# Performance work log

Hardware: AMD Instinct MI355X
Metric: run time of the kernel (lower is better)

The kernel has to match this reference:

```python
import jax, jax.numpy as jnp
import numpy as np

IMAGE_SIZE = 800.0          # torchvision default min_size
SCORE_THRESH = 0.25         # box_score_thresh from __init__
NMS_THRESH = 0.5            # box_nms_thresh from __init__
MAX_DET = 100               # torchvision detections_per_img default
BBOX_XFORM_CLIP = float(np.log(1000.0 / 16.0))  # torchvision BoxCoder clamp


def setup_inputs() -> dict:
    key = jax.random.key(0)
    k = jax.random.split(key, 5)
    B, N, D, C = 16, 4000, 1024, 2
    feats = jax.random.normal(k[0], (B, N, D), dtype=jnp.float32)
    # valid proposal boxes (x1,y1,x2,y2) inside the image
    cxcy = jax.random.uniform(k[1], (B, N, 2), minval=64.0, maxval=IMAGE_SIZE - 64.0)
    wh = jax.random.uniform(k[2], (B, N, 2), minval=16.0, maxval=128.0)
    proposals = jnp.concatenate([cxcy - wh * 0.5, cxcy + wh * 0.5], axis=-1)
    W_cls = jax.random.normal(k[3], (C, D), dtype=jnp.float32) * 0.02
    b_cls = jnp.zeros((C,), jnp.float32)
    W_box = jax.random.normal(k[4], (C * 4, D), dtype=jnp.float32) * 0.01
    b_box = jnp.zeros((C * 4,), jnp.float32)
    return dict(feats=feats, proposals=proposals, W_cls=W_cls, b_cls=b_cls,
                W_box=W_box, b_box=b_box)


def _decode_boxes(deltas, proposals):
    # torchvision BoxCoder with weights (10, 10, 5, 5)
    wx, wy, ww, wh = 10.0, 10.0, 5.0, 5.0
    widths = proposals[..., 2] - proposals[..., 0]
    heights = proposals[..., 3] - proposals[..., 1]
    ctr_x = proposals[..., 0] + 0.5 * widths
    ctr_y = proposals[..., 1] + 0.5 * heights
    dx = deltas[..., 0] / wx
    dy = deltas[..., 1] / wy
    dw = jnp.minimum(deltas[..., 2] / ww, BBOX_XFORM_CLIP)
    dh = jnp.minimum(deltas[..., 3] / wh, BBOX_XFORM_CLIP)
    pcx = dx * widths + ctr_x
    pcy = dy * heights + ctr_y
    pw = jnp.exp(dw) * widths
    ph = jnp.exp(dh) * heights
    boxes = jnp.stack([pcx - 0.5 * pw, pcy - 0.5 * ph,
                       pcx + 0.5 * pw, pcy + 0.5 * ph], axis=-1)
    return jnp.clip(boxes, 0.0, IMAGE_SIZE)


def _nms_keep(boxes, scores):
    # greedy NMS for one image; boxes [N,4], scores [N] (already thresholded)
    areas = jnp.maximum(boxes[:, 2] - boxes[:, 0], 0.0) * \
            jnp.maximum(boxes[:, 3] - boxes[:, 1], 0.0)

    def body(carry, _):
        s, keep = carry
        i = jnp.argmax(s)
        valid = s[i] > 0.0
        bi = boxes[i]
        ix1 = jnp.maximum(bi[0], boxes[:, 0])
        iy1 = jnp.maximum(bi[1], boxes[:, 1])
        ix2 = jnp.minimum(bi[2], boxes[:, 2])
        iy2 = jnp.minimum(bi[3], boxes[:, 3])
        inter = jnp.maximum(ix2 - ix1, 0.0) * jnp.maximum(iy2 - iy1, 0.0)
        iou = inter / (areas[i] + areas - inter + 1e-9)
        s = jnp.where(iou > NMS_THRESH, 0.0, s).at[i].set(0.0)
        keep = keep.at[i].set(valid)
        return (s, keep), None

    init = (scores, jnp.zeros(scores.shape, dtype=bool))
    (_, keep), _ = jax.lax.scan(body, init, None, length=MAX_DET)
    return keep


def reference(feats, proposals, W_cls, b_cls, W_box, b_box):
    logits = jnp.einsum('bnd,cd->bnc', feats, W_cls) + b_cls       # [B,N,2]
    deltas = jnp.einsum('bnd,ed->bne', feats, W_box) + b_box       # [B,N,8]
    probs = jax.nn.softmax(logits, axis=-1)
    scores = probs[..., 1]                                          # foreground class
    fg_deltas = deltas[..., 4:8]                                    # class-1 deltas
    boxes = _decode_boxes(fg_deltas, proposals)                     # [B,N,4]
    scores = jnp.where(scores > SCORE_THRESH, scores, 0.0)
    keep = jax.vmap(_nms_keep)(boxes, scores)                       # [B,N] bool
    final_scores = scores * keep.astype(scores.dtype)
    return jnp.concatenate([boxes, final_scores[..., None]], axis=-1)  # [B,N,5]
```

## Files before the change

### kernel.cpp

```cpp
#include <hip/hip_runtime.h>
#include <math.h>

#define IMG 800.0f
#define SCORE_TH 0.25f
#define NMS_TH 0.5f
#define MAXDET 100
#define BBOX_CLIP 4.135166556742356f

constexpr int kB = 16;
constexpr int kN = 4000;
constexpr int kD = 1024;

__global__ __launch_bounds__(256, 2) void head_kernel(
    const float* __restrict__ feats, const float* __restrict__ proposals,
    const float* __restrict__ Wc, const float* __restrict__ bc,
    const float* __restrict__ Wb, const float* __restrict__ bb,
    float* __restrict__ out, float* __restrict__ ws_scores,
    float* __restrict__ ws_boxes) {
  const int lane = threadIdx.x & 63;
  const int waveId = (blockIdx.x * blockDim.x + threadIdx.x) >> 6;
  const int nWaves = (gridDim.x * blockDim.x) >> 6;

  const float4* Wc4 = (const float4*)Wc;
  const float4* Wb4 = (const float4*)Wb;
  float4 w0[4], w1[4], w4[4], w5[4], w6[4], w7[4];
#pragma unroll
  for (int ch = 0; ch < 4; ++ch) {
    int idx = ch * 64 + lane;
    w0[ch] = Wc4[0 * 256 + idx];
    w1[ch] = Wc4[1 * 256 + idx];
    w4[ch] = Wb4[4 * 256 + idx];
    w5[ch] = Wb4[5 * 256 + idx];
    w6[ch] = Wb4[6 * 256 + idx];
    w7[ch] = Wb4[7 * 256 + idx];
  }
  const float bc0 = bc[0], bc1 = bc[1];
  const float bb4 = bb[4], bb5 = bb[5], bb6 = bb[6], bb7 = bb[7];

  const int R = kB * kN;
  for (int row = waveId; row < R; row += nWaves) {
    const float4* F = (const float4*)(feats + (size_t)row * kD);
    float a0 = 0.f, a1 = 0.f, a4 = 0.f, a5 = 0.f, a6 = 0.f, a7 = 0.f;
#pragma unroll
    for (int ch = 0; ch < 4; ++ch) {
      float4 f = F[ch * 64 + lane];
      a0 = fmaf(f.x, w0[ch].x, fmaf(f.y, w0[ch].y, fmaf(f.z, w0[ch].z, fmaf(f.w, w0[ch].w, a0))));
      a1 = fmaf(f.x, w1[ch].x, fmaf(f.y, w1[ch].y, fmaf(f.z, w1[ch].z, fmaf(f.w, w1[ch].w, a1))));
      a4 = fmaf(f.x, w4[ch].x, fmaf(f.y, w4[ch].y, fmaf(f.z, w4[ch].z, fmaf(f.w, w4[ch].w, a4))));
      a5 = fmaf(f.x, w5[ch].x, fmaf(f.y, w5[ch].y, fmaf(f.z, w5[ch].z, fmaf(f.w, w5[ch].w, a5))));
      a6 = fmaf(f.x, w6[ch].x, fmaf(f.y, w6[ch].y, fmaf(f.z, w6[ch].z, fmaf(f.w, w6[ch].w, a6))));
      a7 = fmaf(f.x, w7[ch].x, fmaf(f.y, w7[ch].y, fmaf(f.z, w7[ch].z, fmaf(f.w, w7[ch].w, a7))));
    }
#pragma unroll
    for (int off = 32; off; off >>= 1) {
      a0 += __shfl_xor(a0, off);
      a1 += __shfl_xor(a1, off);
      a4 += __shfl_xor(a4, off);
      a5 += __shfl_xor(a5, off);
      a6 += __shfl_xor(a6, off);
      a7 += __shfl_xor(a7, off);
    }
    if (lane == 0) {
      float l0 = a0 + bc0, l1 = a1 + bc1;
      float score = 1.0f / (1.0f + __expf(l0 - l1));
      float sth = score > SCORE_TH ? score : 0.0f;

      float4 p = ((const float4*)proposals)[row];
      float w = p.z - p.x, h = p.w - p.y;
      float cx = p.x + 0.5f * w, cy = p.y + 0.5f * h;
      float dx = (a4 + bb4) * 0.1f;
      float dy = (a5 + bb5) * 0.1f;
      float dw = fminf((a6 + bb6) * 0.2f, BBOX_CLIP);
      float dh = fminf((a7 + bb7) * 0.2f, BBOX_CLIP);
      float pcx = fmaf(dx, w, cx), pcy = fmaf(dy, h, cy);
      float pw = __expf(dw) * w, ph = __expf(dh) * h;
      float x1 = fminf(fmaxf(pcx - 0.5f * pw, 0.f), IMG);
      float y1 = fminf(fmaxf(pcy - 0.5f * ph, 0.f), IMG);
      float x2 = fminf(fmaxf(pcx + 0.5f * pw, 0.f), IMG);
      float y2 = fminf(fmaxf(pcy + 0.5f * ph, 0.f), IMG);

      size_t ob = (size_t)row * 5;
      out[ob + 0] = x1;
      out[ob + 1] = y1;
      out[ob + 2] = x2;
      out[ob + 3] = y2;
      ws_scores[row] = sth;
      ((float4*)ws_boxes)[row] = make_float4(x1, y1, x2, y2);
    }
  }
}

template <int CTRL>
__device__ __forceinline__ unsigned long long dpp_max_u64(unsigned long long k) {
  int lo = __builtin_amdgcn_update_dpp(0, (int)(unsigned)k, CTRL, 0xF, 0xF, true);
  int hi =
      __builtin_amdgcn_update_dpp(0, (int)(unsigned)(k >> 32), CTRL, 0xF, 0xF, true);
  unsigned long long o = ((unsigned long long)(unsigned)hi << 32) | (unsigned)lo;
  return o > k ? o : k;
}

__device__ __forceinline__ unsigned long long wave_max_u64(unsigned long long k) {
  k = dpp_max_u64<0x121>(k);
  k = dpp_max_u64<0x122>(k);
  k = dpp_max_u64<0x124>(k);
  k = dpp_max_u64<0x128>(k);
  k = dpp_max_u64<0x142>(k);
  k = dpp_max_u64<0x143>(k);
  return k;
}

__global__ __launch_bounds__(256, 1) void nms_kernel(
    const float* __restrict__ ws_scores, const float* __restrict__ ws_boxes,
    float* __restrict__ out) {
  const int b = blockIdx.x;
  const int t = threadIdx.x;
  const int wave = t >> 6;
  const int lane = t & 63;

  __shared__ float4 Lbox[kN];
  __shared__ unsigned long long Lkey[2][4];

  const float* sc = ws_scores + (size_t)b * kN;
  const float4* bx = (const float4*)ws_boxes + (size_t)b * kN;

  unsigned khi[16];
  float areaE[16];
  float4 box[16];
  unsigned keep_mask = 0u;
  const unsigned nt = ~(unsigned)t;

#pragma unroll
  for (int k = 0; k < 16; ++k) {
    int n = k * 256 + t;
    if (n < kN) {
      box[k] = bx[n];
      khi[k] = __float_as_uint(sc[n]);
      areaE[k] = fmaxf(box[k].z - box[k].x, 0.f) *
                     fmaxf(box[k].w - box[k].y, 0.f) +
                 1e-9f;
      Lbox[n] = box[k];
    } else {
      box[k] = make_float4(0.f, 0.f, 0.f, 0.f);
      khi[k] = 0u;
      areaE[k] = 1e-9f;
    }
  }

  auto reduce_publish = [&](int parity) {
    unsigned long long lk[16];
#pragma unroll
    for (int k = 0; k < 16; ++k)
      lk[k] = ((unsigned long long)khi[k] << 32) |
              (unsigned long long)(nt - (unsigned)(k * 256));
#pragma unroll
    for (int k = 0; k < 8; ++k) lk[k] = lk[k] > lk[k + 8] ? lk[k] : lk[k + 8];
#pragma unroll
    for (int k = 0; k < 4; ++k) lk[k] = lk[k] > lk[k + 4] ? lk[k] : lk[k + 4];
    lk[0] = lk[0] > lk[2] ? lk[0] : lk[2];
    lk[1] = lk[1] > lk[3] ? lk[1] : lk[3];
    lk[0] = lk[0] > lk[1] ? lk[0] : lk[1];
    unsigned long long wkey = wave_max_u64(lk[0]);
    if (lane == 63) Lkey[parity][wave] = wkey;
  };

  reduce_publish(1);
  __syncthreads();

  for (int it = 0; it < MAXDET; ++it) {
    const int pr = (it + 1) & 1;
    unsigned long long wk = Lkey[pr][0];
    unsigned long long k1 = Lkey[pr][1];
    unsigned long long k2 = Lkey[pr][2];
    unsigned long long k3 = Lkey[pr][3];
    wk = wk > k1 ? wk : k1;
    k2 = k2 > k3 ? k2 : k3;
    wk = wk > k2 ? wk : k2;
    const unsigned whi = (unsigned)__builtin_amdgcn_readfirstlane((int)(wk >> 32));
    const unsigned wlo = (unsigned)__builtin_amdgcn_readfirstlane((int)(unsigned)wk);
    const unsigned wn = ~wlo;
    const bool valid = whi != 0u;
    const float4 wb = Lbox[wn];
    const float wa = fmaxf(wb.z - wb.x, 0.f) * fmaxf(wb.w - wb.y, 0.f);
    const bool iOwn = ((unsigned)t == (wn & 255u));
    const int oSlot = (int)(wn >> 8);
    if (iOwn) {
      unsigned bit = 1u << oSlot;
      keep_mask = valid ? (keep_mask | bit) : (keep_mask & ~bit);
    }
#pragma unroll
    for (int k = 0; k < 16; ++k) {
      float dx = fminf(wb.z, box[k].z) - fmaxf(wb.x, box[k].x);
      float dy = fminf(wb.w, box[k].w) - fmaxf(wb.y, box[k].y);
      float inter3 = 3.0f * fmaxf(dx, 0.f) * fmaxf(dy, 0.f);
      bool sup = inter3 > wa + areaE[k];
      if (sup || (iOwn && k == oSlot)) khi[k] = 0u;
    }
    reduce_publish(it & 1);
    __syncthreads();
  }

#pragma unroll
  for (int k = 0; k < 16; ++k) {
    int n = k * 256 + t;
    if (n < kN) {
      out[((size_t)(b * kN + n)) * 5 + 4] =
          (keep_mask >> k) & 1u ? sc[n] : 0.0f;
    }
  }
}

extern "C" void kernel_launch(void* const* d_in, const int* in_sizes, int n_in,
                              void* d_out, int out_size, void* d_ws,
                              size_t ws_size, hipStream_t stream) {
  const float* feats = (const float*)d_in[0];
  const float* proposals = (const float*)d_in[1];
  const float* Wc = (const float*)d_in[2];
  const float* bc = (const float*)d_in[3];
  const float* Wb = (const float*)d_in[4];
  const float* bb = (const float*)d_in[5];
  float* out = (float*)d_out;

  float* ws_scores = (float*)d_ws;
  float* ws_boxes = ws_scores + kB * kN;

  head_kernel<<<512, 256, 0, stream>>>(feats, proposals, Wc, bc, Wb, bb, out,
                                       ws_scores, ws_boxes);
  nms_kernel<<<kB, 256, 0, stream>>>(ws_scores, ws_boxes, out);
}
```

Baseline: 447.0 us.

## Prefetch next feature row in head kernel and widen NMS blocks to 1024 threads

The head kernel now loads the next row's features into registers before computing the current row's dot products, so global-load latency overlaps with the FMA and reduction work. The NMS kernel goes from 256 to 1024 threads per image, so each thread holds 4 box slots instead of 16. That shortens the per-iteration serial IoU loop, at the cost of a 16-way cross-wave key reduction per iteration and a barrier across 16 waves. The prefetch raises register pressure in the head kernel, which may affect its occupancy.

After: 470.5 us. 1.05x slower.

```diff
diff --git a/kernel.cpp b/kernel.cpp
--- a/kernel.cpp
+++ b/kernel.cpp
@@ -38,18 +38,32 @@
   const float bb4 = bb[4], bb5 = bb[5], bb6 = bb[6], bb7 = bb[7];
 
   const int R = kB * kN;
-  for (int row = waveId; row < R; row += nWaves) {
+  int row = waveId;
+  float4 f[4];
+  if (row < R) {
     const float4* F = (const float4*)(feats + (size_t)row * kD);
+#pragma unroll
+    for (int ch = 0; ch < 4; ++ch) f[ch] = F[ch * 64 + lane];
+  }
+  for (; row < R; row += nWaves) {
+    float4 fn[4];
+    const int nrow = row + nWaves;
+    if (nrow < R) {
+      const float4* Fn = (const float4*)(feats + (size_t)nrow * kD);
+#pragma unroll
+      for (int ch = 0; ch < 4; ++ch) fn[ch] = Fn[ch * 64 + lane];
+    }
+
     float a0 = 0.f, a1 = 0.f, a4 = 0.f, a5 = 0.f, a6 = 0.f, a7 = 0.f;
 #pragma unroll
     for (int ch = 0; ch < 4; ++ch) {
-      float4 f = F[ch * 64 + lane];
-      a0 = fmaf(f.x, w0[ch].x, fmaf(f.y, w0[ch].y, fmaf(f.z, w0[ch].z, fmaf(f.w, w0[ch].w, a0))));
-      a1 = fmaf(f.x, w1[ch].x, fmaf(f.y, w1[ch].y, fmaf(f.z, w1[ch].z, fmaf(f.w, w1[ch].w, a1))));
-      a4 = fmaf(f.x, w4[ch].x, fmaf(f.y, w4[ch].y, fmaf(f.z, w4[ch].z, fmaf(f.w, w4[ch].w, a4))));
-      a5 = fmaf(f.x, w5[ch].x, fmaf(f.y, w5[ch].y, fmaf(f.z, w5[ch].z, fmaf(f.w, w5[ch].w, a5))));
-      a6 = fmaf(f.x, w6[ch].x, fmaf(f.y, w6[ch].y, fmaf(f.z, w6[ch].z, fmaf(f.w, w6[ch].w, a6))));
-      a7 = fmaf(f.x, w7[ch].x, fmaf(f.y, w7[ch].y, fmaf(f.z, w7[ch].z, fmaf(f.w, w7[ch].w, a7))));
+      float4 ff = f[ch];
+      a0 = fmaf(ff.x, w0[ch].x, fmaf(ff.y, w0[ch].y, fmaf(ff.z, w0[ch].z, fmaf(ff.w, w0[ch].w, a0))));
+      a1 = fmaf(ff.x, w1[ch].x, fmaf(ff.y, w1[ch].y, fmaf(ff.z, w1[ch].z, fmaf(ff.w, w1[ch].w, a1))));
+      a4 = fmaf(ff.x, w4[ch].x, fmaf(ff.y, w4[ch].y, fmaf(ff.z, w4[ch].z, fmaf(ff.w, w4[ch].w, a4))));
+      a5 = fmaf(ff.x, w5[ch].x, fmaf(ff.y, w5[ch].y, fmaf(ff.z, w5[ch].z, fmaf(ff.w, w5[ch].w, a5))));
+      a6 = fmaf(ff.x, w6[ch].x, fmaf(ff.y, w6[ch].y, fmaf(ff.z, w6[ch].z, fmaf(ff.w, w6[ch].w, a6))));
+      a7 = fmaf(ff.x, w7[ch].x, fmaf(ff.y, w7[ch].y, fmaf(ff.z, w7[ch].z, fmaf(ff.w, w7[ch].w, a7))));
     }
 #pragma unroll
     for (int off = 32; off; off >>= 1) {
@@ -87,6 +101,8 @@
       ws_scores[row] = sth;
       ((float4*)ws_boxes)[row] = make_float4(x1, y1, x2, y2);
     }
+#pragma unroll
+    for (int ch = 0; ch < 4; ++ch) f[ch] = fn[ch];
   }
 }
 
@@ -109,7 +125,11 @@
   return k;
 }
 
-__global__ __launch_bounds__(256, 1) void nms_kernel(
+constexpr int kNmsThreads = 1024;
+constexpr int kSlots = 4;
+constexpr int kNmsWaves = kNmsThreads / 64;
+
+__global__ __launch_bounds__(kNmsThreads, 1) void nms_kernel(
     const float* __restrict__ ws_scores, const float* __restrict__ ws_boxes,
     float* __restrict__ out) {
   const int b = blockIdx.x;
@@ -118,20 +138,20 @@
   const int lane = t & 63;
 
   __shared__ float4 Lbox[kN];
-  __shared__ unsigned long long Lkey[2][4];
+  __shared__ unsigned long long Lkey[2][kNmsWaves];
 
   const float* sc = ws_scores + (size_t)b * kN;
   const float4* bx = (const float4*)ws_boxes + (size_t)b * kN;
 
-  unsigned khi[16];
-  float areaE[16];
-  float4 box[16];
+  unsigned khi[kSlots];
+  float areaE[kSlots];
+  float4 box[kSlots];
   unsigned keep_mask = 0u;
   const unsigned nt = ~(unsigned)t;
 
 #pragma unroll
-  for (int k = 0; k < 16; ++k) {
-    int n = k * 256 + t;
+  for (int k = 0; k < kSlots; ++k) {
+    int n = k * kNmsThreads + t;
     if (n < kN) {
       box[k] = bx[n];
       khi[k] = __float_as_uint(sc[n]);
@@ -147,15 +167,11 @@
   }
 
   auto reduce_publish = [&](int parity) {
-    unsigned long long lk[16];
-#pragma unroll
-    for (int k = 0; k < 16; ++k)
+    unsigned long long lk[kSlots];
+#pragma unroll
+    for (int k = 0; k < kSlots; ++k)
       lk[k] = ((unsigned long long)khi[k] << 32) |
-              (unsigned long long)(nt - (unsigned)(k * 256));
-#pragma unroll
-    for (int k = 0; k < 8; ++k) lk[k] = lk[k] > lk[k + 8] ? lk[k] : lk[k + 8];
-#pragma unroll
-    for (int k = 0; k < 4; ++k) lk[k] = lk[k] > lk[k + 4] ? lk[k] : lk[k + 4];
+              (unsigned long long)(nt - (unsigned)(k * kNmsThreads));
     lk[0] = lk[0] > lk[2] ? lk[0] : lk[2];
     lk[1] = lk[1] > lk[3] ? lk[1] : lk[3];
     lk[0] = lk[0] > lk[1] ? lk[0] : lk[1];
@@ -168,27 +184,31 @@
 
   for (int it = 0; it < MAXDET; ++it) {
     const int pr = (it + 1) & 1;
-    unsigned long long wk = Lkey[pr][0];
-    unsigned long long k1 = Lkey[pr][1];
-    unsigned long long k2 = Lkey[pr][2];
-    unsigned long long k3 = Lkey[pr][3];
-    wk = wk > k1 ? wk : k1;
-    k2 = k2 > k3 ? k2 : k3;
-    wk = wk > k2 ? wk : k2;
+    unsigned long long m[8];
+#pragma unroll
+    for (int i = 0; i < 8; ++i) {
+      unsigned long long a = Lkey[pr][i], c = Lkey[pr][i + 8];
+      m[i] = a > c ? a : c;
+    }
+#pragma unroll
+    for (int i = 0; i < 4; ++i) m[i] = m[i] > m[i + 4] ? m[i] : m[i + 4];
+    m[0] = m[0] > m[2] ? m[0] : m[2];
+    m[1] = m[1] > m[3] ? m[1] : m[3];
+    unsigned long long wk = m[0] > m[1] ? m[0] : m[1];
     const unsigned whi = (unsigned)__builtin_amdgcn_readfirstlane((int)(wk >> 32));
     const unsigned wlo = (unsigned)__builtin_amdgcn_readfirstlane((int)(unsigned)wk);
     const unsigned wn = ~wlo;
     const bool valid = whi != 0u;
     const float4 wb = Lbox[wn];
     const float wa = fmaxf(wb.z - wb.x, 0.f) * fmaxf(wb.w - wb.y, 0.f);
-    const bool iOwn = ((unsigned)t == (wn & 255u));
-    const int oSlot = (int)(wn >> 8);
+    const bool iOwn = ((unsigned)t == (wn & (unsigned)(kNmsThreads - 1)));
+    const int oSlot = (int)(wn >> 10);
     if (iOwn) {
       unsigned bit = 1u << oSlot;
       keep_mask = valid ? (keep_mask | bit) : (keep_mask & ~bit);
     }
 #pragma unroll
-    for (int k = 0; k < 16; ++k) {
+    for (int k = 0; k < kSlots; ++k) {
       float dx = fminf(wb.z, box[k].z) - fmaxf(wb.x, box[k].x);
       float dy = fminf(wb.w, box[k].w) - fmaxf(wb.y, box[k].y);
       float inter3 = 3.0f * fmaxf(dx, 0.f) * fmaxf(dy, 0.f);
@@ -200,8 +220,8 @@
   }
 
 #pragma unroll
-  for (int k = 0; k < 16; ++k) {
-    int n = k * 256 + t;
+  for (int k = 0; k < kSlots; ++k) {
+    int n = k * kNmsThreads + t;
     if (n < kN) {
       out[((size_t)(b * kN + n)) * 5 + 4] =
           (keep_mask >> k) & 1u ? sc[n] : 0.0f;
@@ -225,5 +245,5 @@
 
   head_kernel<<<512, 256, 0, stream>>>(feats, proposals, Wc, bc, Wb, bb, out,
                                        ws_scores, ws_boxes);
-  nms_kernel<<<kB, 256, 0, stream>>>(ws_scores, ws_boxes, out);
-}
+  nms_kernel<<<kB, kNmsThreads, 0, stream>>>(ws_scores, ws_boxes, out);
+}
```
